# Optimization experiments

Measured on AMD Instinct MI355X. Metric: run time of the kernel, lower is better.

Reference implementation:

```python
import jax, jax.numpy as jnp
import numpy as np
from jax import lax

G = 32          # growthrate / num_features
KS = 3          # filter_size
PAD = (KS - 1) // 2
NUM_LAYERS = 4


def _conv2d(x, w, b):
    # x: [B, Cin, H, W], w: [Cout, Cin, k, k]
    y = lax.conv_general_dilated(
        x, w, window_strides=(1, 1), padding=[(PAD, PAD), (PAD, PAD)],
        dimension_numbers=("NCHW", "OIHW", "NCHW"))
    return y + b[None, :, None, None]


def _scan_cell(xs, w, b):
    # xs: [T, B, Cin, H, W]; ConvLSTM-like cell: A = tanh(conv(cat(x, c)))
    # split A -> (ai[G], af[G], ao[1]); h = ai; c_next = sigmoid(ao) * af
    T, B, _, H, W = xs.shape
    c0 = jnp.zeros((B, G, H, W), xs.dtype)

    def step(c, x):
        A = jnp.tanh(_conv2d(jnp.concatenate([x, c], axis=1), w, b))
        h = A[:, :G]
        cand = A[:, G:2 * G]
        gate = jax.nn.sigmoid(A[:, 2 * G:])
        c_next = gate * cand
        return c_next, (h, c_next, gate)

    _, (hs, cs, gs) = lax.scan(step, c0, xs)
    return hs, cs, gs  # each [T, B, G or 1, H, W]


def setup_inputs() -> dict:
    key = jax.random.key(0)
    ks = jax.random.split(key, 1 + 4 * NUM_LAYERS)
    T, B, C, H, W = 8, 4, 32, 64, 64
    inp = {"x": jax.random.normal(ks[0], (T, B, C, H, W), jnp.float32)}
    cin = [C] + [2 * l * G for l in range(1, NUM_LAYERS)]  # [32, 64, 128, 192]
    cout = 2 * G + 1
    for l in range(NUM_LAYERS):
        ci = cin[l] + G
        inp[f"wf{l}"] = jax.random.normal(ks[1 + 4 * l], (cout, ci, KS, KS), jnp.float32) * 0.02
        inp[f"bf{l}"] = jax.random.normal(ks[2 + 4 * l], (cout,), jnp.float32) * 0.02
        inp[f"wb{l}"] = jax.random.normal(ks[3 + 4 * l], (cout, ci, KS, KS), jnp.float32) * 0.02
        inp[f"bb{l}"] = jax.random.normal(ks[4 + 4 * l], (cout,), jnp.float32) * 0.02
    return inp


def reference(x, wf0, bf0, wb0, bb0, wf1, bf1, wb1, bb1,
              wf2, bf2, wb2, bb2, wf3, bf3, wb3, bb3):
    fwd = [(wf0, bf0), (wf1, bf1), (wf2, bf2), (wf3, bf3)]
    bwd = [(wb0, bb0), (wb1, bb1), (wb2, bb2), (wb3, bb3)]
    output = x  # [T, B, C, H, W]
    lr_h, lr_c, lr_g = [], [], []
    for l in range(NUM_LAYERS):
        hf, cf, gf = _scan_cell(output, *fwd[l])
        hb, _, _ = _scan_cell(output[::-1], *bwd[l])
        hb = hb[::-1]  # align backward pass to original time order
        cur = jnp.concatenate([hf, hb], axis=2)  # [T, B, 2G, H, W]
        output = cur if l == 0 else jnp.concatenate([output, cur], axis=2)
        lr_h.append(hf[-1]); lr_c.append(cf[-1]); lr_g.append(gf[-1])
    return (output, jnp.stack(lr_h), jnp.stack(lr_c), jnp.stack(lr_g))
```

## Files before the change

### kernel.cpp

```cpp
#include <hip/hip_runtime.h>
#include <math.h>

#define T_STEPS 8
#define HW 4096
#define XSTR 192
#define FR_ROW 4352

typedef unsigned short u16;
typedef __attribute__((ext_vector_type(8))) short short8;
typedef __attribute__((ext_vector_type(4))) short short4v;
typedef __attribute__((ext_vector_type(4))) float f32x4;

__device__ __forceinline__ u16 f2bf(float f) {
    unsigned u = __builtin_bit_cast(unsigned, f);
    u += 0x7fffu + ((u >> 16) & 1u);
    return (u16)(u >> 16);
}
__device__ __forceinline__ float bf2f(u16 h) {
    unsigned u = ((unsigned)h) << 16;
    return __builtin_bit_cast(float, u);
}
__device__ __forceinline__ float ftanh(float x) {
    float e = __expf(2.f * x);
    return 1.f - 2.f * __builtin_amdgcn_rcpf(e + 1.f);
}
__device__ __forceinline__ float fsigm(float x) {
    return __builtin_amdgcn_rcpf(1.f + __expf(-x));
}

__global__ __launch_bounds__(256) void transpose_halo(
    const float* __restrict__ src, u16* __restrict__ XT, int src_ctot)
{
    __shared__ float tile[32][257];
    const int img = blockIdx.z;
    const int px0 = blockIdx.x * 256;
    const float* s = src + (size_t)img * src_ctot * HW + px0;
    #pragma unroll
    for (int c = 0; c < 32; ++c)
        tile[c][threadIdx.x] = s[(size_t)c * HW + threadIdx.x];
    __syncthreads();
    const int c = threadIdx.x & 31, pb = threadIdx.x >> 5;
    const int r0 = px0 >> 6;
    for (int p = pb; p < 256; p += 8) {
        int row = r0 + (p >> 6), col = p & 63;
        XT[((size_t)img * 4356 + (row + 1) * 66 + col + 1) * XSTR + c] = f2bf(tile[c][p]);
    }
}

struct WP { const float* p[8]; };

__global__ __launch_bounds__(256) void prep_w_all(WP wp, u16* __restrict__ Wr)
{
    int idx = blockIdx.x * 256 + threadIdx.x;
    if (idx >= 783360) return;
    const int offs[5] = {0, 92160, 230400, 460800, 783360};
    const int cit[4]  = {64, 96, 160, 224};
    int lay = 0;
    while (idx >= offs[lay + 1]) ++lay;
    int li = idx - offs[lay];
    int ci_total = cit[lay];
    int ci = li % ci_total;
    int rest = li / ci_total;
    int co = rest % 80; rest /= 80;
    int tap = rest % 9;
    int dir = rest / 9;
    const float* w = wp.p[lay * 2 + dir];
    float v = (co < 65) ? w[((size_t)co * ci_total + ci) * 9 + tap] : 0.f;
    Wr[idx] = f2bf(v);
}

__global__ __launch_bounds__(512, 2) void convx_mfma(
    const u16* __restrict__ XT, const u16* __restrict__ Wr,
    const float* __restrict__ b_f, const float* __restrict__ b_b,
    u16* __restrict__ convx, int cin, int ci_total)
{
    __shared__ u16 xs[6 * 66 * 32];
    const int tid = threadIdx.x;
    const int l = tid & 63, wv = tid >> 6;
    const int g = l >> 4, ln16 = l & 15;
    const int img = blockIdx.z;
    const int dir = wv & 1;
    const int wrow = wv >> 1;
    const int r0  = blockIdx.x * 4;
    const int orow = r0 + wrow;

    const float* bias = dir ? b_b : b_f;
    f32x4 acc[5][4];
    #pragma unroll
    for (int mt = 0; mt < 5; ++mt)
        #pragma unroll
        for (int r = 0; r < 4; ++r) {
            int co = mt * 16 + g * 4 + r;
            float bv = (co < 65) ? bias[co] : 0.f;
            #pragma unroll
            for (int nt = 0; nt < 4; ++nt) acc[mt][nt][r] = bv;
        }

    const u16* wdir = Wr + (size_t)dir * 9 * 80 * ci_total + g * 8;
    const u16* xim  = XT + (size_t)img * 4356 * XSTR;

    for (int ch = 0; ch < cin; ch += 32) {
        __syncthreads();
        #pragma unroll
        for (int k = 0; k < 4; ++k) {
            int idx = k * 512 + tid;
            if (idx < 1584) {
                int seg = idx & 3;
                int pr  = idx >> 2;
                short8 v = *(const short8*)(xim + (size_t)(r0 * 66 + pr) * XSTR + ch + seg * 8);
                *(short8*)(xs + (size_t)idx * 8) = v;
            }
        }
        __syncthreads();

        #pragma unroll
        for (int ky = 0; ky < 3; ++ky) {
            #pragma unroll
            for (int kx = 0; kx < 3; ++kx) {
                const int tap = ky * 3 + kx;
                const u16* xb = xs + ((size_t)((wrow + ky) * 66 + ln16 + kx)) * 32 + g * 8;
                short8 bv0 = *(const short8*)(xb);
                short8 bv1 = *(const short8*)(xb + 16 * 32);
                short8 bv2 = *(const short8*)(xb + 32 * 32);
                short8 bv3 = *(const short8*)(xb + 48 * 32);
                const u16* wb_ = wdir + ((size_t)tap * 80 + ln16) * ci_total + ch;
                #pragma unroll
                for (int mt = 0; mt < 5; ++mt) {
                    short8 af = *(const short8*)(wb_ + (size_t)mt * 16 * ci_total);
                    acc[mt][0] = __builtin_amdgcn_mfma_f32_16x16x32_bf16(af, bv0, acc[mt][0], 0, 0, 0);
                    acc[mt][1] = __builtin_amdgcn_mfma_f32_16x16x32_bf16(af, bv1, acc[mt][1], 0, 0, 0);
                    acc[mt][2] = __builtin_amdgcn_mfma_f32_16x16x32_bf16(af, bv2, acc[mt][2], 0, 0, 0);
                    acc[mt][3] = __builtin_amdgcn_mfma_f32_16x16x32_bf16(af, bv3, acc[mt][3], 0, 0, 0);
                }
            }
        }
    }

    const int zimg = dir * 32 + img;
    u16* cb = convx + ((size_t)zimg * 64 + orow) * FR_ROW;
    #pragma unroll
    for (int mt = 0; mt < 4; ++mt)
        #pragma unroll
        for (int nt = 0; nt < 4; ++nt) {
            short4v pk;
            #pragma unroll
            for (int r = 0; r < 4; ++r) pk[r] = (short)f2bf(acc[mt][nt][r]);
            *(short4v*)(cb + (size_t)(nt * 4 + mt) * 256 + l * 4) = pk;
        }
    if (g == 0) {
        #pragma unroll
        for (int nt = 0; nt < 4; ++nt) {
            short4v pk;
            #pragma unroll
            for (int r = 0; r < 4; ++r) pk[r] = (short)f2bf(acc[4][nt][r]);
            *(short4v*)(cb + 4096 + nt * 64 + ln16 * 4) = pk;
        }
    }
}

__global__ __launch_bounds__(512) void rec_mfma(
    const u16* __restrict__ cT_in, u16* __restrict__ cT_out,
    const u16* __restrict__ Wr, const u16* __restrict__ convx,
    float* __restrict__ out_t,
    float* __restrict__ lrh, float* __restrict__ lrc, float* __restrict__ lrg,
    u16* __restrict__ XT,
    int cin, int ci_total, int layer, int step)
{
    const int tid = threadIdx.x;
    const int l = tid & 63, w = tid >> 6;
    const int g = l >> 4, ln16 = l & 15;
    const int role = w & 1, ws = w >> 1;
    const int z = blockIdx.z;
    const int dir = z >> 2, b = z & 3;
    const int t = dir ? (7 - step) : step;
    const int row  = blockIdx.x * 2 + (ws >> 1);
    const int nb   = (ws & 1) * 2;
    const int col0 = nb * 16;
    const int zimg = dir * 32 + t * 4 + b;
    const int m0 = role * 2;

    const u16* cxb = convx + ((size_t)zimg * 64 + row) * FR_ROW;
    short4v cx[3][2];
    #pragma unroll
    for (int j = 0; j < 2; ++j)
        #pragma unroll
        for (int nt = 0; nt < 2; ++nt)
            cx[j][nt] = *(const short4v*)(cxb + (size_t)((nb + nt) * 4 + (m0 + j)) * 256 + l * 4);
    #pragma unroll
    for (int nt = 0; nt < 2; ++nt)
        cx[2][nt] = (g == 0)
            ? *(const short4v*)(cxb + 4096 + (nb + nt) * 64 + ln16 * 4)
            : (short4v){0, 0, 0, 0};

    f32x4 acc[3][2] = {};
    if (step > 0) {
        const u16* wdir = Wr + (size_t)dir * 9 * 80 * ci_total + cin + g * 8;
        const u16* cim  = cT_in + (size_t)z * 4356 * 32 + g * 8;
        __builtin_amdgcn_s_setprio(1);
        #pragma unroll
        for (int ky = 0; ky < 3; ++ky) {
            #pragma unroll
            for (int kx = 0; kx < 3; ++kx) {
                const int tap = ky * 3 + kx;
                const u16* xb_ = cim + (size_t)((row + ky) * 66 + col0 + ln16 + kx) * 32;
                short8 bv0 = *(const short8*)(xb_);
                short8 bv1 = *(const short8*)(xb_ + 16 * 32);
                const u16* wb_ = wdir + ((size_t)tap * 80 + ln16) * ci_total;
                short8 af0 = *(const short8*)(wb_ + (size_t)(m0    ) * 16 * ci_total);
                short8 af1 = *(const short8*)(wb_ + (size_t)(m0 + 1) * 16 * ci_total);
                short8 af4 = *(const short8*)(wb_ + (size_t)4 * 16 * ci_total);
                acc[0][0] = __builtin_amdgcn_mfma_f32_16x16x32_bf16(af0, bv0, acc[0][0], 0, 0, 0);
                acc[0][1] = __builtin_amdgcn_mfma_f32_16x16x32_bf16(af0, bv1, acc[0][1], 0, 0, 0);
                acc[1][0] = __builtin_amdgcn_mfma_f32_16x16x32_bf16(af1, bv0, acc[1][0], 0, 0, 0);
                acc[1][1] = __builtin_amdgcn_mfma_f32_16x16x32_bf16(af1, bv1, acc[1][1], 0, 0, 0);
                acc[2][0] = __builtin_amdgcn_mfma_f32_16x16x32_bf16(af4, bv0, acc[2][0], 0, 0, 0);
                acc[2][1] = __builtin_amdgcn_mfma_f32_16x16x32_bf16(af4, bv1, acc[2][1], 0, 0, 0);
            }
        }
        __builtin_amdgcn_s_setprio(0);
    }

    const bool last_f = (dir == 0) && (step == 7);
    float val[2], gv[2];
    #pragma unroll
    for (int nt = 0; nt < 2; ++nt) {
        val[nt] = fsigm(ftanh(acc[2][nt][0] + bf2f((u16)cx[2][nt][0])));
        gv[nt]  = __shfl(val[nt], ln16);
    }

    if (role == 0) {
        const size_t obase = (size_t)(t * 4 + b) * 256 + 64 * layer + dir * 32;
        const int chb = 64 * layer + dir * 32;
        #pragma unroll
        for (int j = 0; j < 2; ++j)
            #pragma unroll
            for (int nt = 0; nt < 2; ++nt) {
                int px = row * 64 + col0 + nt * 16 + ln16;
                short4v pkh;
                #pragma unroll
                for (int r = 0; r < 4; ++r) {
                    int co = j * 16 + g * 4 + r;
                    float v = ftanh(acc[j][nt][r] + bf2f((u16)cx[j][nt][r]));
                    out_t[(obase + co) * HW + px] = v;
                    pkh[r] = (short)f2bf(v);
                    if (last_f) lrh[((size_t)(layer * 4 + b) * 32 + co) * HW + px] = v;
                }
                if (layer < 3)
                    *(short4v*)(XT + ((size_t)(t * 4 + b) * 4356 + (row + 1) * 66 +
                                      (col0 + nt * 16 + ln16 + 1)) * XSTR + chb + j * 16 + g * 4) = pkh;
            }
        if (last_f && g == 0) {
            #pragma unroll
            for (int nt = 0; nt < 2; ++nt)
                lrg[(size_t)(layer * 4 + b) * HW + row * 64 + col0 + nt * 16 + ln16] = val[nt];
        }
    } else {
        #pragma unroll
        for (int j = 0; j < 2; ++j)
            #pragma unroll
            for (int nt = 0; nt < 2; ++nt) {
                short4v pk;
                #pragma unroll
                for (int r = 0; r < 4; ++r) {
                    int k = j * 16 + g * 4 + r;
                    float c = gv[nt] * ftanh(acc[j][nt][r] + bf2f((u16)cx[j][nt][r]));
                    pk[r] = (short)f2bf(c);
                    if (last_f)
                        lrc[((size_t)(layer * 4 + b) * 32 + k) * HW + row * 64 + col0 + nt * 16 + ln16] = c;
                }
                if (step < 7) {
                    int colh = col0 + nt * 16 + ln16 + 1;
                    *(short4v*)(cT_out + ((size_t)z * 4356 + (row + 1) * 66 + colh) * 32 + j * 16 + g * 4) = pk;
                }
            }
    }
}

extern "C" void kernel_launch(void* const* d_in, const int* in_sizes, int n_in,
                              void* d_out, int out_size, void* d_ws, size_t ws_size,
                              hipStream_t stream)
{
    const float* x = (const float*)d_in[0];
    float* out = (float*)d_out;
    float* lrh = out + (size_t)33554432;
    float* lrc = lrh + (size_t)2097152;
    float* lrg = lrc + (size_t)2097152;

    char* ws = (char*)d_ws;
    u16* convx = (u16*)ws;
    size_t off = 35651584 + 4096;
    u16* cT_a = (u16*)(ws + off); off += 2230272;
    u16* cT_b = (u16*)(ws + off); off += 2230272;
    u16* XT = (u16*)(ws + off); off += 53526528;
    u16* Wr = (u16*)(ws + off);

    static const int offs[4] = {0, 92160, 230400, 460800};

    hipMemsetAsync(XT, 0, 53526528, stream);
    hipMemsetAsync(cT_a, 0, 2230272, stream);
    hipMemsetAsync(cT_b, 0, 2230272, stream);
    transpose_halo<<<dim3(16, 1, 32), 256, 0, stream>>>(x, XT, 32);

    WP wp;
    for (int l = 0; l < 4; ++l) {
        wp.p[l * 2]     = (const float*)d_in[1 + 4 * l];
        wp.p[l * 2 + 1] = (const float*)d_in[3 + 4 * l];
    }
    prep_w_all<<<dim3((783360 + 255) / 256), 256, 0, stream>>>(wp, Wr);

    for (int l = 0; l < 4; ++l) {
        const float* bf = (const float*)d_in[2 + 4 * l];
        const float* bb = (const float*)d_in[4 + 4 * l];
        int cin = (l == 0) ? 32 : 64 * l;
        int ci_total = cin + 32;
        const u16* Wrl = Wr + offs[l];

        convx_mfma<<<dim3(16, 1, 32), 512, 0, stream>>>(XT, Wrl, bf, bb, convx, cin, ci_total);

        for (int s = 0; s < 8; ++s) {
            const u16* cin_p = (s & 1) ? cT_b : cT_a;
            u16* cout_p      = (s & 1) ? cT_a : cT_b;
            rec_mfma<<<dim3(32, 1, 8), 512, 0, stream>>>(
                cin_p, cout_p, Wrl, convx, out, lrh, lrc, lrg, XT,
                cin, ci_total, l, s);
        }
    }
}
```

Baseline: 576.6 us.

## Split input-conv channel reduction across two blocks and zero only XT halo

The input convolution for layers 1-3 is split along the input-channel reduction into two grid slices (gridDim.y=2), each writing partial sums to a separate convx buffer. The recurrent kernel adds both partials before the activations. This doubles the number of blocks (512 to 1024), which is meant to fill more CUs, at the cost of extra workspace, extra partial-sum writes and reads, and double bf16 rounding of the partials. The full memset of XT is also replaced by a small kernel that zeroes only the halo border.

```diff
diff --git a/kernel.cpp b/kernel.cpp
--- a/kernel.cpp
+++ b/kernel.cpp
@@ -5,6 +5,7 @@
 #define HW 4096
 #define XSTR 192
 #define FR_ROW 4352
+#define CVBUF 17825792
 
 typedef unsigned short u16;
 typedef __attribute__((ext_vector_type(8))) short short8;
@@ -45,6 +46,23 @@
         int row = r0 + (p >> 6), col = p & 63;
         XT[((size_t)img * 4356 + (row + 1) * 66 + col + 1) * XSTR + c] = f2bf(tile[c][p]);
     }
+}
+
+__global__ __launch_bounds__(256) void zero_border(u16* __restrict__ XT)
+{
+    int idx = blockIdx.x * 256 + threadIdx.x;
+    if (idx >= 199680) return;
+    int c8 = idx % 24;
+    int rest = idx / 24;
+    int bp = rest % 260;
+    int img = rest / 260;
+    int row, col;
+    if (bp < 66)       { row = 0;  col = bp; }
+    else if (bp < 132) { row = 65; col = bp - 66; }
+    else if (bp < 196) { col = 0;  row = 1 + bp - 132; }
+    else               { col = 65; row = 1 + bp - 196; }
+    short8 zz = {0, 0, 0, 0, 0, 0, 0, 0};
+    *(short8*)(XT + ((size_t)img * 4356 + row * 66 + col) * XSTR + c8 * 8) = zz;
 }
 
 struct WP { const float* p[8]; };
@@ -72,17 +90,20 @@
 __global__ __launch_bounds__(512, 2) void convx_mfma(
     const u16* __restrict__ XT, const u16* __restrict__ Wr,
     const float* __restrict__ b_f, const float* __restrict__ b_b,
-    u16* __restrict__ convx, int cin, int ci_total)
+    u16* __restrict__ convx, int cin, int ci_total, int split_ch)
 {
     __shared__ u16 xs[6 * 66 * 32];
     const int tid = threadIdx.x;
     const int l = tid & 63, wv = tid >> 6;
     const int g = l >> 4, ln16 = l & 15;
     const int img = blockIdx.z;
+    const int y = blockIdx.y;
     const int dir = wv & 1;
     const int wrow = wv >> 1;
     const int r0  = blockIdx.x * 4;
     const int orow = r0 + wrow;
+    const int cbeg = (y == 0) ? 0 : split_ch;
+    const int cend = (y == 0 && gridDim.y == 2) ? split_ch : cin;
 
     const float* bias = dir ? b_b : b_f;
     f32x4 acc[5][4];
@@ -91,7 +112,7 @@
         #pragma unroll
         for (int r = 0; r < 4; ++r) {
             int co = mt * 16 + g * 4 + r;
-            float bv = (co < 65) ? bias[co] : 0.f;
+            float bv = (y == 0 && co < 65) ? bias[co] : 0.f;
             #pragma unroll
             for (int nt = 0; nt < 4; ++nt) acc[mt][nt][r] = bv;
         }
@@ -99,7 +120,7 @@
     const u16* wdir = Wr + (size_t)dir * 9 * 80 * ci_total + g * 8;
     const u16* xim  = XT + (size_t)img * 4356 * XSTR;
 
-    for (int ch = 0; ch < cin; ch += 32) {
+    for (int ch = cbeg; ch < cend; ch += 32) {
         __syncthreads();
         #pragma unroll
         for (int k = 0; k < 4; ++k) {
@@ -137,7 +158,7 @@
     }
 
     const int zimg = dir * 32 + img;
-    u16* cb = convx + ((size_t)zimg * 64 + orow) * FR_ROW;
+    u16* cb = convx + (size_t)y * CVBUF + ((size_t)zimg * 64 + orow) * FR_ROW;
     #pragma unroll
     for (int mt = 0; mt < 4; ++mt)
         #pragma unroll
@@ -164,7 +185,7 @@
     float* __restrict__ out_t,
     float* __restrict__ lrh, float* __restrict__ lrc, float* __restrict__ lrg,
     u16* __restrict__ XT,
-    int cin, int ci_total, int layer, int step)
+    int cin, int ci_total, int layer, int step, int split)
 {
     const int tid = threadIdx.x;
     const int l = tid & 63, w = tid >> 6;
@@ -180,17 +201,22 @@
     const int m0 = role * 2;
 
     const u16* cxb = convx + ((size_t)zimg * 64 + row) * FR_ROW;
-    short4v cx[3][2];
+    const u16* cxb1 = cxb + CVBUF;
+    short4v cx0[3][2], cx1[3][2];
     #pragma unroll
     for (int j = 0; j < 2; ++j)
         #pragma unroll
-        for (int nt = 0; nt < 2; ++nt)
-            cx[j][nt] = *(const short4v*)(cxb + (size_t)((nb + nt) * 4 + (m0 + j)) * 256 + l * 4);
-    #pragma unroll
-    for (int nt = 0; nt < 2; ++nt)
-        cx[2][nt] = (g == 0)
-            ? *(const short4v*)(cxb + 4096 + (nb + nt) * 64 + ln16 * 4)
-            : (short4v){0, 0, 0, 0};
+        for (int nt = 0; nt < 2; ++nt) {
+            size_t o = (size_t)((nb + nt) * 4 + (m0 + j)) * 256 + l * 4;
+            cx0[j][nt] = *(const short4v*)(cxb + o);
+            cx1[j][nt] = split ? *(const short4v*)(cxb1 + o) : (short4v){0, 0, 0, 0};
+        }
+    #pragma unroll
+    for (int nt = 0; nt < 2; ++nt) {
+        size_t o = 4096 + (size_t)(nb + nt) * 64 + ln16 * 4;
+        cx0[2][nt] = (g == 0) ? *(const short4v*)(cxb + o) : (short4v){0, 0, 0, 0};
+        cx1[2][nt] = (g == 0 && split) ? *(const short4v*)(cxb1 + o) : (short4v){0, 0, 0, 0};
+    }
 
     f32x4 acc[3][2] = {};
     if (step > 0) {
@@ -224,7 +250,7 @@
     float val[2], gv[2];
     #pragma unroll
     for (int nt = 0; nt < 2; ++nt) {
-        val[nt] = fsigm(ftanh(acc[2][nt][0] + bf2f((u16)cx[2][nt][0])));
+        val[nt] = fsigm(ftanh(acc[2][nt][0] + bf2f((u16)cx0[2][nt][0]) + bf2f((u16)cx1[2][nt][0])));
         gv[nt]  = __shfl(val[nt], ln16);
     }
 
@@ -240,7 +266,7 @@
                 #pragma unroll
                 for (int r = 0; r < 4; ++r) {
                     int co = j * 16 + g * 4 + r;
-                    float v = ftanh(acc[j][nt][r] + bf2f((u16)cx[j][nt][r]));
+                    float v = ftanh(acc[j][nt][r] + bf2f((u16)cx0[j][nt][r]) + bf2f((u16)cx1[j][nt][r]));
                     out_t[(obase + co) * HW + px] = v;
                     pkh[r] = (short)f2bf(v);
                     if (last_f) lrh[((size_t)(layer * 4 + b) * 32 + co) * HW + px] = v;
@@ -263,7 +289,7 @@
                 #pragma unroll
                 for (int r = 0; r < 4; ++r) {
                     int k = j * 16 + g * 4 + r;
-                    float c = gv[nt] * ftanh(acc[j][nt][r] + bf2f((u16)cx[j][nt][r]));
+                    float c = gv[nt] * ftanh(acc[j][nt][r] + bf2f((u16)cx0[j][nt][r]) + bf2f((u16)cx1[j][nt][r]));
                     pk[r] = (short)f2bf(c);
                     if (last_f)
                         lrc[((size_t)(layer * 4 + b) * 32 + k) * HW + row * 64 + col0 + nt * 16 + ln16] = c;
@@ -287,16 +313,22 @@
     float* lrg = lrc + (size_t)2097152;
 
     char* ws = (char*)d_ws;
-    u16* convx = (u16*)ws;
-    size_t off = 35651584 + 4096;
+    const size_t NEEDED = 130861056;
+    const bool split_ok = ws_size >= NEEDED;
+
+    size_t off = 0;
+    u16* convx = (u16*)ws; off += (size_t)CVBUF * 2;
+    if (split_ok) off += (size_t)CVBUF * 2;
+    off += 4096;
     u16* cT_a = (u16*)(ws + off); off += 2230272;
     u16* cT_b = (u16*)(ws + off); off += 2230272;
     u16* XT = (u16*)(ws + off); off += 53526528;
     u16* Wr = (u16*)(ws + off);
 
     static const int offs[4] = {0, 92160, 230400, 460800};
-
-    hipMemsetAsync(XT, 0, 53526528, stream);
+    static const int splitc[4] = {0, 32, 64, 96};
+
+    zero_border<<<dim3(780), 256, 0, stream>>>(XT);
     hipMemsetAsync(cT_a, 0, 2230272, stream);
     hipMemsetAsync(cT_b, 0, 2230272, stream);
     transpose_halo<<<dim3(16, 1, 32), 256, 0, stream>>>(x, XT, 32);
@@ -314,15 +346,17 @@
         int cin = (l == 0) ? 32 : 64 * l;
         int ci_total = cin + 32;
         const u16* Wrl = Wr + offs[l];
-
-        convx_mfma<<<dim3(16, 1, 32), 512, 0, stream>>>(XT, Wrl, bf, bb, convx, cin, ci_total);
+        const int ksplit = (split_ok && l > 0) ? 2 : 1;
+
+        convx_mfma<<<dim3(16, ksplit, 32), 512, 0, stream>>>(
+            XT, Wrl, bf, bb, convx, cin, ci_total, splitc[l]);
 
         for (int s = 0; s < 8; ++s) {
             const u16* cin_p = (s & 1) ? cT_b : cT_a;
             u16* cout_p      = (s & 1) ? cT_a : cT_b;
             rec_mfma<<<dim3(32, 1, 8), 512, 0, stream>>>(
                 cin_p, cout_p, Wrl, convx, out, lrh, lrc, lrg, XT,
-                cin, ci_total, l, s);
-        }
-    }
-}
+                cin, ci_total, l, s, ksplit - 1);
+        }
+    }
+}
```

Measured after the change: 614.3 us. 6.5% more time.

## Split recurrent tile across 16 waves and zero only XT halo borders

Applied to the files above, without the earlier changes.

The recurrent kernel now runs 1024 threads per block, and each wave computes a single 16-channel output group plus the gate, where before each wave computed two groups. This doubles the wave-level parallelism on the serial per-step critical path but duplicates the gate MFMAs and the weight/input loads in every wave. Separately, the full memset of the 53 MB XT buffer is replaced by a kernel that zeroes only the halo border pixels, since every interior pixel is written later anyway. This relies on all interior channels actually being written before they are read.

```diff
diff --git a/kernel.cpp b/kernel.cpp
--- a/kernel.cpp
+++ b/kernel.cpp
@@ -45,6 +45,23 @@
         int row = r0 + (p >> 6), col = p & 63;
         XT[((size_t)img * 4356 + (row + 1) * 66 + col + 1) * XSTR + c] = f2bf(tile[c][p]);
     }
+}
+
+__global__ __launch_bounds__(256) void zero_border(u16* __restrict__ XT)
+{
+    int idx = blockIdx.x * 256 + threadIdx.x;
+    if (idx >= 199680) return;
+    int c8 = idx % 24;
+    int rest = idx / 24;
+    int bp = rest % 260;
+    int img = rest / 260;
+    int row, col;
+    if (bp < 66)       { row = 0;  col = bp; }
+    else if (bp < 132) { row = 65; col = bp - 66; }
+    else if (bp < 196) { col = 0;  row = 1 + bp - 132; }
+    else               { col = 65; row = 1 + bp - 196; }
+    short8 zz = {0, 0, 0, 0, 0, 0, 0, 0};
+    *(short8*)(XT + ((size_t)img * 4356 + row * 66 + col) * XSTR + c8 * 8) = zz;
 }
 
 struct WP { const float* p[8]; };
@@ -158,7 +175,7 @@
     }
 }
 
-__global__ __launch_bounds__(512) void rec_mfma(
+__global__ __launch_bounds__(1024) void rec_mfma(
     const u16* __restrict__ cT_in, u16* __restrict__ cT_out,
     const u16* __restrict__ Wr, const u16* __restrict__ convx,
     float* __restrict__ out_t,
@@ -169,7 +186,7 @@
     const int tid = threadIdx.x;
     const int l = tid & 63, w = tid >> 6;
     const int g = l >> 4, ln16 = l & 15;
-    const int role = w & 1, ws = w >> 1;
+    const int role = w & 3, ws = w >> 2;
     const int z = blockIdx.z;
     const int dir = z >> 2, b = z & 3;
     const int t = dir ? (7 - step) : step;
@@ -177,22 +194,18 @@
     const int nb   = (ws & 1) * 2;
     const int col0 = nb * 16;
     const int zimg = dir * 32 + t * 4 + b;
-    const int m0 = role * 2;
 
     const u16* cxb = convx + ((size_t)zimg * 64 + row) * FR_ROW;
-    short4v cx[3][2];
-    #pragma unroll
-    for (int j = 0; j < 2; ++j)
-        #pragma unroll
-        for (int nt = 0; nt < 2; ++nt)
-            cx[j][nt] = *(const short4v*)(cxb + (size_t)((nb + nt) * 4 + (m0 + j)) * 256 + l * 4);
-    #pragma unroll
-    for (int nt = 0; nt < 2; ++nt)
-        cx[2][nt] = (g == 0)
-            ? *(const short4v*)(cxb + 4096 + (nb + nt) * 64 + ln16 * 4)
+    short4v cxo[2], cxg[2];
+    #pragma unroll
+    for (int nt = 0; nt < 2; ++nt) {
+        cxo[nt] = *(const short4v*)(cxb + (size_t)((nb + nt) * 4 + role) * 256 + l * 4);
+        cxg[nt] = (g == 0)
+            ? *(const short4v*)(cxb + 4096 + (size_t)(nb + nt) * 64 + ln16 * 4)
             : (short4v){0, 0, 0, 0};
-
-    f32x4 acc[3][2] = {};
+    }
+
+    f32x4 accO[2] = {}, accG[2] = {};
     if (step > 0) {
         const u16* wdir = Wr + (size_t)dir * 9 * 80 * ci_total + cin + g * 8;
         const u16* cim  = cT_in + (size_t)z * 4356 * 32 + g * 8;
@@ -206,15 +219,12 @@
                 short8 bv0 = *(const short8*)(xb_);
                 short8 bv1 = *(const short8*)(xb_ + 16 * 32);
                 const u16* wb_ = wdir + ((size_t)tap * 80 + ln16) * ci_total;
-                short8 af0 = *(const short8*)(wb_ + (size_t)(m0    ) * 16 * ci_total);
-                short8 af1 = *(const short8*)(wb_ + (size_t)(m0 + 1) * 16 * ci_total);
+                short8 afO = *(const short8*)(wb_ + (size_t)role * 16 * ci_total);
                 short8 af4 = *(const short8*)(wb_ + (size_t)4 * 16 * ci_total);
-                acc[0][0] = __builtin_amdgcn_mfma_f32_16x16x32_bf16(af0, bv0, acc[0][0], 0, 0, 0);
-                acc[0][1] = __builtin_amdgcn_mfma_f32_16x16x32_bf16(af0, bv1, acc[0][1], 0, 0, 0);
-                acc[1][0] = __builtin_amdgcn_mfma_f32_16x16x32_bf16(af1, bv0, acc[1][0], 0, 0, 0);
-                acc[1][1] = __builtin_amdgcn_mfma_f32_16x16x32_bf16(af1, bv1, acc[1][1], 0, 0, 0);
-                acc[2][0] = __builtin_amdgcn_mfma_f32_16x16x32_bf16(af4, bv0, acc[2][0], 0, 0, 0);
-                acc[2][1] = __builtin_amdgcn_mfma_f32_16x16x32_bf16(af4, bv1, acc[2][1], 0, 0, 0);
+                accO[0] = __builtin_amdgcn_mfma_f32_16x16x32_bf16(afO, bv0, accO[0], 0, 0, 0);
+                accO[1] = __builtin_amdgcn_mfma_f32_16x16x32_bf16(afO, bv1, accO[1], 0, 0, 0);
+                accG[0] = __builtin_amdgcn_mfma_f32_16x16x32_bf16(af4, bv0, accG[0], 0, 0, 0);
+                accG[1] = __builtin_amdgcn_mfma_f32_16x16x32_bf16(af4, bv1, accG[1], 0, 0, 0);
             }
         }
         __builtin_amdgcn_s_setprio(0);
@@ -224,55 +234,52 @@
     float val[2], gv[2];
     #pragma unroll
     for (int nt = 0; nt < 2; ++nt) {
-        val[nt] = fsigm(ftanh(acc[2][nt][0] + bf2f((u16)cx[2][nt][0])));
+        val[nt] = fsigm(ftanh(accG[nt][0] + bf2f((u16)cxg[nt][0])));
         gv[nt]  = __shfl(val[nt], ln16);
     }
 
-    if (role == 0) {
+    if (role < 2) {
         const size_t obase = (size_t)(t * 4 + b) * 256 + 64 * layer + dir * 32;
         const int chb = 64 * layer + dir * 32;
         #pragma unroll
-        for (int j = 0; j < 2; ++j)
-            #pragma unroll
-            for (int nt = 0; nt < 2; ++nt) {
-                int px = row * 64 + col0 + nt * 16 + ln16;
-                short4v pkh;
-                #pragma unroll
-                for (int r = 0; r < 4; ++r) {
-                    int co = j * 16 + g * 4 + r;
-                    float v = ftanh(acc[j][nt][r] + bf2f((u16)cx[j][nt][r]));
-                    out_t[(obase + co) * HW + px] = v;
-                    pkh[r] = (short)f2bf(v);
-                    if (last_f) lrh[((size_t)(layer * 4 + b) * 32 + co) * HW + px] = v;
-                }
-                if (layer < 3)
-                    *(short4v*)(XT + ((size_t)(t * 4 + b) * 4356 + (row + 1) * 66 +
-                                      (col0 + nt * 16 + ln16 + 1)) * XSTR + chb + j * 16 + g * 4) = pkh;
-            }
-        if (last_f && g == 0) {
+        for (int nt = 0; nt < 2; ++nt) {
+            int px = row * 64 + col0 + nt * 16 + ln16;
+            short4v pkh;
+            #pragma unroll
+            for (int r = 0; r < 4; ++r) {
+                int co = role * 16 + g * 4 + r;
+                float v = ftanh(accO[nt][r] + bf2f((u16)cxo[nt][r]));
+                out_t[(obase + co) * HW + px] = v;
+                pkh[r] = (short)f2bf(v);
+                if (last_f) lrh[((size_t)(layer * 4 + b) * 32 + co) * HW + px] = v;
+            }
+            if (layer < 3)
+                *(short4v*)(XT + ((size_t)(t * 4 + b) * 4356 + (row + 1) * 66 +
+                                  (col0 + nt * 16 + ln16 + 1)) * XSTR + chb + role * 16 + g * 4) = pkh;
+        }
+        if (last_f && role == 0 && g == 0) {
             #pragma unroll
             for (int nt = 0; nt < 2; ++nt)
                 lrg[(size_t)(layer * 4 + b) * HW + row * 64 + col0 + nt * 16 + ln16] = val[nt];
         }
     } else {
         #pragma unroll
-        for (int j = 0; j < 2; ++j)
-            #pragma unroll
-            for (int nt = 0; nt < 2; ++nt) {
-                short4v pk;
-                #pragma unroll
-                for (int r = 0; r < 4; ++r) {
-                    int k = j * 16 + g * 4 + r;
-                    float c = gv[nt] * ftanh(acc[j][nt][r] + bf2f((u16)cx[j][nt][r]));
-                    pk[r] = (short)f2bf(c);
-                    if (last_f)
-                        lrc[((size_t)(layer * 4 + b) * 32 + k) * HW + row * 64 + col0 + nt * 16 + ln16] = c;
-                }
-                if (step < 7) {
-                    int colh = col0 + nt * 16 + ln16 + 1;
-                    *(short4v*)(cT_out + ((size_t)z * 4356 + (row + 1) * 66 + colh) * 32 + j * 16 + g * 4) = pk;
-                }
-            }
+        for (int nt = 0; nt < 2; ++nt) {
+            short4v pk;
+            #pragma unroll
+            for (int r = 0; r < 4; ++r) {
+                int k = (role - 2) * 16 + g * 4 + r;
+                float c = gv[nt] * ftanh(accO[nt][r] + bf2f((u16)cxo[nt][r]));
+                pk[r] = (short)f2bf(c);
+                if (last_f)
+                    lrc[((size_t)(layer * 4 + b) * 32 + k) * HW + row * 64 + col0 + nt * 16 + ln16] = c;
+            }
+            if (step < 7) {
+                int colh = col0 + nt * 16 + ln16 + 1;
+                *(short4v*)(cT_out + ((size_t)z * 4356 + (row + 1) * 66 + colh) * 32 +
+                            (role - 2) * 16 + g * 4) = pk;
+            }
+        }
     }
 }
 
@@ -296,7 +303,7 @@
 
     static const int offs[4] = {0, 92160, 230400, 460800};
 
-    hipMemsetAsync(XT, 0, 53526528, stream);
+    zero_border<<<dim3(780), 256, 0, stream>>>(XT);
     hipMemsetAsync(cT_a, 0, 2230272, stream);
     hipMemsetAsync(cT_b, 0, 2230272, stream);
     transpose_halo<<<dim3(16, 1, 32), 256, 0, stream>>>(x, XT, 32);
@@ -320,7 +327,7 @@
         for (int s = 0; s < 8; ++s) {
             const u16* cin_p = (s & 1) ? cT_b : cT_a;
             u16* cout_p      = (s & 1) ? cT_a : cT_b;
-            rec_mfma<<<dim3(32, 1, 8), 512, 0, stream>>>(
+            rec_mfma<<<dim3(32, 1, 8), 1024, 0, stream>>>(
                 cin_p, cout_p, Wrl, convx, out, lrh, lrc, lrg, XT,
                 cin, ci_total, l, s);
         }
```

Result: slower. 647.6 us (+12.3%).
